# Performance work log

Hardware: AMD Instinct MI355X
Metric: run time of the kernel (lower is better)

The kernel has to match this reference:

```python
import jax, jax.numpy as jnp
import numpy as np

GAMMA = 5.0 / 3.0
SG = float(np.sqrt(GAMMA - 1.0))
NC, E, H = 1000000, 5, 32

def _csnd(rho, p):
    h = 1.0 + GAMMA / (GAMMA - 1.0) * p / rho
    return jnp.sqrt(GAMMA * p / (rho * h))

def _vstar_from_cs(cs, cs_a, v_a, wave_sign):
    # Marti-Muller relativistic rarefaction Riemann invariant
    ratio = ((SG - cs) / (SG + cs)) * ((SG + cs_a) / (SG - cs_a))
    A = ((1.0 + v_a) / (1.0 - v_a)) * ratio ** (-wave_sign * 2.0 / SG)
    return (A - 1.0) / (A + 1.0)

def _get_vel_raref(p, rho_a, p_a, v_a, wave_sign):
    rho = rho_a * (p / p_a) ** (1.0 / GAMMA)          # isentrope
    h = 1.0 + GAMMA / (GAMMA - 1.0) * p / rho
    cs = jnp.sqrt(GAMMA * p / (rho * h))
    vstar = _vstar_from_cs(cs, _csnd(rho_a, p_a), v_a, wave_sign)
    W = 1.0 / jnp.sqrt(1.0 - vstar ** 2)
    return rho, p / rho, h, cs, vstar, W

def _raref_solver(prims, sign):
    # state inside the rarefaction fan at xi = x/t = 0: v = sign*cs
    rho_a, p_a, v_a = prims[:, 0], prims[:, 1], prims[:, 2]
    cs_a = _csnd(rho_a, p_a)
    wave_sign = -float(sign)
    f = lambda cs: _vstar_from_cs(cs, cs_a, v_a, wave_sign) - sign * cs
    lo = jnp.full_like(rho_a, 1e-6)
    hi = jnp.full_like(rho_a, SG - 1e-6)
    flo = f(lo)
    for _ in range(40):  # fixed-count bisection, jit-safe
        mid = 0.5 * (lo + hi)
        fm = f(mid)
        same = jnp.sign(fm) == jnp.sign(flo)
        lo = jnp.where(same, mid, lo)
        flo = jnp.where(same, fm, flo)
        hi = jnp.where(same, hi, mid)
    cs = 0.5 * (lo + hi)
    h = (GAMMA - 1.0) / (GAMMA - 1.0 - cs ** 2)
    k = (h - 1.0) * (GAMMA - 1.0) / GAMMA              # p / rho
    rho = (k * rho_a ** GAMMA / p_a) ** (1.0 / (GAMMA - 1.0))
    return rho, k * rho, h, sign * cs

def setup_inputs():
    key = jax.random.key(0)
    ks = jax.random.split(key, 10)
    rho = 0.5 + jax.random.uniform(ks[0], (NC, 1, 2))
    p = 0.5 + jax.random.uniform(ks[1], (NC, 1, 2))
    v = 0.8 * (jax.random.uniform(ks[2], (NC, 1, 2)) - 0.5)
    P = jnp.concatenate([rho, p, v], axis=1)           # (NC,3,2)
    U = jax.random.normal(ks[3], (NC, 3, 2))
    F = jax.random.normal(ks[4], (NC, 3, 2))
    cmax = jax.random.uniform(ks[5], (NC,))
    cmin = -jax.random.uniform(ks[6], (NC,))
    s = lambda fan: 0.5 / np.sqrt(fan)
    W1 = jax.random.normal(ks[7], (E, H, 6)) * s(6)
    b1 = jnp.zeros((E, H))
    W2 = jax.random.normal(ks[8], (E, H, H)) * s(H)
    b2 = jnp.zeros((E, H))
    W3 = jax.random.normal(ks[9], (E, 1, H)) * s(H)
    b3 = jnp.zeros((E, 1))
    return {"P": P, "U": U, "F": F, "cmax": cmax, "cmin": cmin,
            "W1": W1, "b1": b1, "W2": W2, "b2": b2, "W3": W3, "b3": b3}

def _forward(P, U, F, cmax, cmin, W1, b1, W2, b2, W3, b3):
    rhoL, rhoR = P[:, 0, 0], P[:, 0, 1]
    pL, pR = P[:, 1, 0], P[:, 1, 1]
    vL, vR = P[:, 2, 0], P[:, 2, 1]
    # pressnet ensemble, batched over E instead of a Python loop
    x = jnp.concatenate([jnp.log(P[:, 0]), jnp.log(P[:, 1]), P[:, 2]], axis=1)  # (NC,6)
    h1 = jnp.tanh(jnp.einsum('nf,ehf->neh', x, W1) + b1)
    h2 = jnp.tanh(jnp.einsum('neh,egh->neg', h1, W2) + b2)
    xi = jax.nn.sigmoid(jnp.einsum('neh,eoh->neo', h2, W3) + b3)[..., 0]        # (NC,E)
    pressC = xi * jnp.minimum(pL, pR)[:, None]        # affine compactification [0, min(pL,pR)]
    rhoCLe, _, hCLe, csCLe, vstarLe, _ = _get_vel_raref(pressC, rhoL[:, None], pL[:, None], vL[:, None], -1.0)
    rhoCRe, _, hCRe, csCRe, vstarRe, _ = _get_vel_raref(pressC, rhoR[:, None], pR[:, None], vR[:, None], +1.0)
    best = jnp.argmin(jnp.abs(vstarLe - vstarRe), axis=1)
    pick = lambda a: jnp.take_along_axis(a, best[:, None], axis=1)[:, 0]
    pressCs = pick(pressC)
    rhoCL, hCL, csCL, vstarL = pick(rhoCLe), pick(hCLe), pick(csCLe), pick(vstarLe)
    rhoCR, hCR, csCR, vstarR = pick(rhoCRe), pick(hCRe), pick(csCRe), pick(vstarRe)
    csL, csR = _csnd(rhoL, pL), _csnd(rhoR, pR)
    lambdaC = 0.5 * (vstarR + vstarL)
    lambdaRL = (lambdaC - csCL) / (1.0 - lambdaC * csCL)
    lambdaL = (vL - csL) / (1.0 - vL * csL)
    lambdaRR = (lambdaC + csCR) / (1.0 + lambdaC * csCR)
    lambdaR = (vR + csR) / (1.0 + vR * csR)
    WC = 1.0 / jnp.sqrt(1.0 - lambdaC ** 2)
    densCL, densCR = WC * rhoCL, WC * rhoCR
    momCL = WC ** 2 * rhoCL * hCL * lambdaC
    momCR = WC ** 2 * rhoCR * hCR * lambdaC
    FCL = jnp.stack([densCL * lambdaC, densCL * (WC * hCL - 1.0) * lambdaC, momCL * lambdaC + pressCs], axis=1)
    FCR = jnp.stack([densCR * lambdaC, densCR * (WC * hCR - 1.0) * lambdaC, momCR * lambdaC + pressCs], axis=1)
    rho_RL, p_RL, h_RL, v_RL = _raref_solver(P[:, :3, 0], +1.0)
    rho_RR, p_RR, h_RR, v_RR = _raref_solver(P[:, :3, 1], -1.0)
    WRL = 1.0 / jnp.sqrt(1.0 - v_RL ** 2)
    WRR = 1.0 / jnp.sqrt(1.0 - v_RR ** 2)
    densRL, densRR = WRL * rho_RL, WRR * rho_RR
    momRL = WRL ** 2 * rho_RL * h_RL * v_RL
    momRR = WRR ** 2 * rho_RR * h_RR * v_RR
    FRL = jnp.stack([densRL * v_RL, densRL * (WRL * h_RL - 1.0) * v_RL, momRL * v_RL + p_RL], axis=1)
    FRR = jnp.stack([densRR * v_RR, densRR * (WRR * h_RR - 1.0) * v_RR, momRR * v_RR + p_RR], axis=1)
    fluxes = jnp.zeros_like(F[:, :, 0])
    sel = lambda m, val, cur: jnp.where(m[:, None], val, cur)
    fluxes = sel(lambdaL >= 0, F[:, :, 0], fluxes)
    fluxes = sel((lambdaL < 0) & (lambdaRL >= 0), FRL, fluxes)
    fluxes = sel((lambdaRL < 0) & (lambdaC > 0), FCL, fluxes)
    fluxes = sel((lambdaC <= 0) & (lambdaRR > 0), FCR, fluxes)
    fluxes = sel((lambdaRR <= 0) & (lambdaR > 0), FRR, fluxes)
    fluxes = sel(lambdaR <= 0, F[:, :, 1], fluxes)
    return fluxes

def reference(P, U, F, cmax, cmin, W1, b1, W2, b2, W3, b3):
    return _forward(P, U, F, cmax, cmin, W1, b1, W2, b2, W3, b3)
```

## Files before the change

kernel.cpp:

```cpp
#include <hip/hip_runtime.h>
#include <hip/hip_bf16.h>
#include <math.h>
#include <stdint.h>

namespace {

constexpr int NE  = 5;
constexpr int NH  = 32;
constexpr int BLK = 256;
constexpr int WPB = BLK / 64;

typedef __attribute__((ext_vector_type(8))) _Float16 half8;
typedef __attribute__((ext_vector_type(2))) __fp16   fp16x2;
typedef __attribute__((ext_vector_type(4))) float    f32x4;

union U4H8 { uint4 u; half8 h; };
union U1H2 { uint32_t u; fp16x2 h; };

__device__ __forceinline__ float bflo(uint32_t u){ return __uint_as_float(u << 16); }
__device__ __forceinline__ float bfhi(uint32_t u){ return __uint_as_float(u & 0xffff0000u); }
__device__ __forceinline__ float b2f(uint16_t u){ return __uint_as_float(((uint32_t)u) << 16); }

constexpr float GAM   = (float)(5.0 / 3.0);
constexpr float G1    = (float)(2.0 / 3.0);
constexpr float CP    = 2.5f;
constexpr float SGc   = (float)0.81649658092772603;
constexpr float E2SG  = (float)2.4494897427831781;
constexpr float LOG2E = 1.4426950408889634f;
constexpr float TLG   = 2.0f * LOG2E;

__device__ __forceinline__ float fexp2(float x){ return __builtin_amdgcn_exp2f(x); }
__device__ __forceinline__ float flog2(float x){ return __builtin_amdgcn_logf(x); }
__device__ __forceinline__ float frcp (float x){ return __builtin_amdgcn_rcpf(x); }
__device__ __forceinline__ float frsq (float x){ return __builtin_amdgcn_rsqf(x); }
__device__ __forceinline__ float fdiv (float a, float b){ return a * frcp(b); }

__device__ __forceinline__ float csnd_fast(float rho, float p){
    return sqrtf(GAM * p * frcp(rho + CP * p));
}

__device__ __forceinline__ uint32_t pk16(float a, float b){
    U1H2 x; x.h = __builtin_amdgcn_cvt_pkrtz(a, b); return x.u;
}
__device__ __forceinline__ uint32_t pkrtn(float a, float b){
    union { _Float16 h[2]; uint32_t u; } cv;
    cv.h[0] = (_Float16)a; cv.h[1] = (_Float16)b;
    return cv.u;
}

__device__ __forceinline__ int kxr(int r){ return (r ^ (r >> 2)) & 3; }

template<bool F32>
__device__ __forceinline__ float wload(const void* p, int idx){
    if constexpr (F32) return ((const float*)p)[idx];
    else               return b2f(((const uint16_t*)p)[idx]);
}

__device__ __forceinline__ void binv8(const float d[8], float i[8]){
    float P1 = d[0] * d[1], P2 = P1 * d[2], P3 = P2 * d[3];
    float P4 = P3 * d[4], P5 = P4 * d[5], P6 = P5 * d[6], P7 = P6 * d[7];
    float R = frcp(P7);
    i[7] = R * P6; R *= d[7];
    i[6] = R * P5; R *= d[6];
    i[5] = R * P4; R *= d[5];
    i[4] = R * P3; R *= d[4];
    i[3] = R * P2; R *= d[3];
    i[2] = R * P1; R *= d[2];
    i[1] = R * d[0];
    i[0] = R * d[1];
}

__device__ __forceinline__ void raref_solver2(float l2rhoL_, float pL_, float kNL,
                                              float l2rhoR_, float pR_, float kNR,
                                              float& rhoRL, float& pRL, float& hRL, float& vRL,
                                              float& rhoRR, float& pRR, float& hRR, float& vRR)
{
    float loL = 1e-6f, hiL = SGc - 1e-6f, csL = 0.40f;
    float loR = 1e-6f, hiR = SGc - 1e-6f, csR = 0.40f;
    #pragma unroll 1
    for(int it = 0; it < 12; ++it){
        float aL = SGc + csL, aR = SGc + csR;
        float Pa = aL * aR, Ra = frcp(Pa);
        float lrL = flog2((SGc - csL) * (Ra * aR));
        float lrR = flog2((SGc - csR) * (Ra * aL));
        float bL = 1.0f - csL, bR = 1.0f - csR;
        float Pb = bL * bR, Rb = frcp(Pb);
        float a2L = flog2((1.0f + csL) * (Rb * bR));
        float a2R = flog2((1.0f + csR) * (Rb * bL));
        float gL = fmaf(E2SG, lrL, kNL) - a2L;
        float gR = fmaf(-E2SG, lrR, kNR) + a2R;
        float d1L = (SGc - csL) * aL, d2L = bL * (1.0f + csL);
        float d1R = (SGc - csR) * aR, d2R = bR * (1.0f + csR);
        float numL = LOG2E * (-2.0f * SGc * E2SG * d2L - 2.0f * d1L);
        float numR = LOG2E * ( 2.0f * SGc * E2SG * d2R + 2.0f * d1R);
        float Pn = numL * numR, Rn = frcp(Pn);
        float csnL = csL - gL * d1L * d2L * (Rn * numR);
        float csnR = csR - gR * d1R * d2R * (Rn * numL);
        bool abL = (gL > 0.0f);
        bool abR = (gR < 0.0f);
        loL = abL ? csL : loL;  hiL = abL ? hiL : csL;
        loR = abR ? csR : loR;  hiR = abR ? hiR : csR;
        csnL = (csnL > loL && csnL < hiL) ? csnL : 0.5f * (loL + hiL);
        csnR = (csnR > loR && csnR < hiR) ? csnR : 0.5f * (loR + hiR);
        bool conv = (fabsf(csnL - csL) < 2e-7f) && (fabsf(csnR - csR) < 2e-7f);
        csL = csnL; csR = csnR;
        if(__all(conv)) break;
    }
    float e1L = G1 - csL * csL, e1R = G1 - csR * csR;
    float Pe = e1L * e1R, Re = frcp(Pe);
    hRL = G1 * (Re * e1R);  hRR = G1 * (Re * e1L);
    float kL = (hRL - 1.0f) * 0.4f, kR = (hRR - 1.0f) * 0.4f;
    float Pp = pL_ * pR_, Rp = frcp(Pp);
    float baseL = kL * fexp2(GAM * l2rhoL_) * (Rp * pR_);
    float baseR = kR * fexp2(GAM * l2rhoR_) * (Rp * pL_);
    rhoRL = baseL * sqrtf(baseL);
    rhoRR = baseR * sqrtf(baseR);
    pRL = kL * rhoRL;  pRR = kR * rhoRR;
    vRL = csL;  vRR = -csR;
}

template<bool F32>
__device__ __forceinline__ void cell_block(const void* Pp, const void* Fp,
                                           const void* W1p, const void* b1p,
                                           const void* W2p, const void* b2p,
                                           const void* W3p, const void* b3p,
                                           float* __restrict__ out, int nc,
                                           uint32_t* Hu ,
                                           uint32_t* sW1u ,
                                           uint32_t* sW2u ,
                                           float* sB1, float* sB2, float* sW3, float* sC)
{
    const int lane = threadIdx.x & 63;
    const int l16  = lane & 15;
    const int quad = lane >> 4;
    const int k16  = kxr(l16);
    const int sw   = quad ^ k16;

    for(int i = threadIdx.x; i < NE * NH * 16; i += BLK){
        int row = i >> 4, kp = i & 15;
        float f0 = wload<F32>(W2p, row * NH + 2 * kp) * TLG;
        float f1 = wload<F32>(W2p, row * NH + 2 * kp + 1) * TLG;
        int idx = (row << 4) | ((((kp >> 2) ^ kxr(row)) << 2) | (kp & 3));
        sW2u[idx] = pkrtn(f0, f1);
    }
    for(int i = threadIdx.x; i < NE * NH * 4; i += BLK){
        int row = i >> 2, kp = i & 3;
        int k0 = 2 * kp, k1 = 2 * kp + 1;
        float f0 = (k0 < 6) ? wload<F32>(W1p, row * 6 + k0) * ((k0 < 4) ? 2.0f : TLG) : 0.0f;
        float f1 = (k1 < 6) ? wload<F32>(W1p, row * 6 + k1) * ((k1 < 4) ? 2.0f : TLG) : 0.0f;
        sW1u[i] = pkrtn(f0, f1);
    }
    for(int i = threadIdx.x; i < NE * NH; i += BLK){
        sB1[i] = wload<F32>(b1p, i) * TLG;
        sB2[i] = wload<F32>(b2p, i) * TLG;
        sW3[i] = wload<F32>(W3p, i) * (-LOG2E);
    }
    if(threadIdx.x < NE){
        float s = wload<F32>(b3p, threadIdx.x) * (-LOG2E);
        for(int j = 0; j < NH; ++j)
            s += wload<F32>(W3p, threadIdx.x * NH + j) * (-LOG2E);
        sC[threadIdx.x] = s;
    }
    __syncthreads();

    const int n  = blockIdx.x * BLK + threadIdx.x;
    const bool valid = (n < nc);
    const int nn = valid ? n : 0;

    float rhoL, rhoR, pL, pR, vL, vR;
    if constexpr (F32){
        const float2* Pf = (const float2*)((const float*)Pp + (size_t)nn * 6);
        float2 a = Pf[0], b = Pf[1], c = Pf[2];
        rhoL = a.x; rhoR = a.y; pL = b.x; pR = b.y; vL = c.x; vR = c.y;
    } else {
        const uint32_t* P32 = (const uint32_t*)Pp;
        uint32_t pa = P32[nn * 3 + 0], pb = P32[nn * 3 + 1], pc = P32[nn * 3 + 2];
        rhoL = bflo(pa); rhoR = bfhi(pa);
        pL   = bflo(pb); pR   = bfhi(pb);
        vL   = bflo(pc); vR   = bfhi(pc);
    }

    float l2rhoL = flog2(rhoL), l2rhoR = flog2(rhoR);
    float l2pL   = flog2(pL),   l2pR   = flog2(pR);

    float csL = csnd_fast(rhoL, pL);
    float csR = csnd_fast(rhoR, pR);
    float pmin = fminf(pL, pR);
    float l2pmin = fminf(l2pL, l2pR);

    float lnraL = flog2((SGc + csL) * frcp(SGc - csL));
    float lnraR = flog2((SGc + csR) * frcp(SGc - csR));
    float lnvL  = flog2((1.0f + vL) * frcp(1.0f - vL));
    float lnvR  = flog2((1.0f + vR) * frcp(1.0f - vR));

    float kNL = fmaf( E2SG, lnraL, lnvL);
    float kNR = fmaf(-E2SG, lnraR, lnvR);

    float c6L = 0.6f * l2pL - l2rhoL;
    float c6R = 0.6f * l2pR - l2rhoR;
    float dLR = fexp2(c6R - c6L);

    U4H8 Bx[4];
    {
        uint32_t x01 = pk16(l2rhoL, l2rhoR);
        uint32_t x23 = pk16(l2pL, l2pR);
        uint32_t x45 = pk16(vL, vR);
        *(uint4*)&Hu[(lane << 4) + (k16 << 2)] = make_uint4(x01, x23, x45, 0u);
        #pragma unroll
        for(int t = 0; t < 4; ++t){
            uint4 b = *(const uint4*)&Hu[((t * 16 + l16) << 4) + (kxr(l16) << 2)];
            Bx[t].u = (quad == 0) ? b : make_uint4(0u, 0u, 0u, 0u);
        }
    }

    float bestd = 1e30f;
    float xaW = 0.f, porL = 1.f, csCL = 0.f, vstarL = 0.f;
    float porR = 1.f, csCR = 0.f, vstarR = 0.f;

    const int cpos0 = (((quad >> 1) ^ k16) << 2) + ((quad & 1) << 1);
    const int cpos1 = (((2 + (quad >> 1)) ^ k16) << 2) + ((quad & 1) << 1);

    #pragma unroll 1
    for(int e = 0; e < NE; ++e){
        U4H8 A1[2];
        #pragma unroll
        for(int m2 = 0; m2 < 2; ++m2){
            uint4 w = *(const uint4*)&sW1u[(e * NH + m2 * 16 + l16) << 2];
            A1[m2].u = (quad == 0) ? w : make_uint4(0u, 0u, 0u, 0u);
        }

        f32x4 acc1[2][4];
        #pragma unroll
        for(int m2 = 0; m2 < 2; ++m2){
            f32x4 bias = *(const f32x4*)&sB1[e * NH + m2 * 16 + quad * 4];
            #pragma unroll
            for(int t = 0; t < 4; ++t) acc1[m2][t] = bias;
        }
        #pragma unroll
        for(int t = 0; t < 4; ++t)
            #pragma unroll
            for(int m2 = 0; m2 < 2; ++m2)
                acc1[m2][t] = __builtin_amdgcn_mfma_f32_16x16x32_f16(A1[m2].h, Bx[t].h, acc1[m2][t], 0, 0, 0);

        #pragma unroll
        for(int t = 0; t < 4; ++t){
            float dv[8], iv[8];
            #pragma unroll
            for(int m2 = 0; m2 < 2; ++m2)
                #pragma unroll
                for(int r = 0; r < 4; ++r)
                    dv[m2 * 4 + r] = fexp2(acc1[m2][t][r]) + 1.0f;
            binv8(dv, iv);
            int c = t * 16 + l16;
            uint32_t u0 = pk16(fmaf(-2.0f, iv[0], 1.0f), fmaf(-2.0f, iv[1], 1.0f));
            uint32_t u1 = pk16(fmaf(-2.0f, iv[2], 1.0f), fmaf(-2.0f, iv[3], 1.0f));
            uint32_t u2 = pk16(fmaf(-2.0f, iv[4], 1.0f), fmaf(-2.0f, iv[5], 1.0f));
            uint32_t u3 = pk16(fmaf(-2.0f, iv[6], 1.0f), fmaf(-2.0f, iv[7], 1.0f));
            *(uint2*)&Hu[(c << 4) + cpos0] = make_uint2(u0, u1);
            *(uint2*)&Hu[(c << 4) + cpos1] = make_uint2(u2, u3);
        }

        U4H8 Ah[2];
        #pragma unroll
        for(int m2 = 0; m2 < 2; ++m2)
            Ah[m2].u = *(const uint4*)&sW2u[((e * NH + m2 * 16 + l16) << 4) + (sw << 2)];

        f32x4 acc[2][4];
        #pragma unroll
        for(int m2 = 0; m2 < 2; ++m2){
            f32x4 bias = *(const f32x4*)&sB2[e * NH + m2 * 16 + quad * 4];
            #pragma unroll
            for(int t = 0; t < 4; ++t) acc[m2][t] = bias;
        }

        #pragma unroll
        for(int t = 0; t < 4; ++t){
            int cell = t * 16 + l16;
            U4H8 Bh;
            Bh.u = *(const uint4*)&Hu[(cell << 4) + (sw << 2)];
            #pragma unroll
            for(int m2 = 0; m2 < 2; ++m2)
                acc[m2][t] = __builtin_amdgcn_mfma_f32_16x16x32_f16(Ah[m2].h, Bh.h, acc[m2][t], 0, 0, 0);
        }

        f32x4 w3v[2];
        #pragma unroll
        for(int m2 = 0; m2 < 2; ++m2)
            w3v[m2] = *(const f32x4*)&sW3[e * NH + m2 * 16 + quad * 4];
        float part[4];
        #pragma unroll
        for(int t = 0; t < 4; ++t){
            float dv[8], iv[8];
            #pragma unroll
            for(int m2 = 0; m2 < 2; ++m2)
                #pragma unroll
                for(int r = 0; r < 4; ++r)
                    dv[m2 * 4 + r] = fexp2(acc[m2][t][r]) + 1.0f;
            binv8(dv, iv);
            float s = 0.0f;
            #pragma unroll
            for(int m2 = 0; m2 < 2; ++m2)
                #pragma unroll
                for(int r = 0; r < 4; ++r)
                    s = fmaf(w3v[m2][r], iv[m2 * 4 + r], s);
            s += __shfl_xor(s, 16, 64);
            s += __shfl_xor(s, 32, 64);
            part[t] = s;
        }
        float p01 = (lane & 16) ? part[1] : part[0];
        float p23 = (lane & 16) ? part[3] : part[2];
        float partS = (lane & 32) ? p23 : p01;
        float xa = fmaf(-2.0f, partS, sC[e]);

        float E = fexp2(xa);
        float l2pC = l2pmin - flog2(1.0f + E);

        float porL_ = fexp2(fmaf(0.4f, l2pC, c6L));
        float porR_ = porL_ * dLR;
        float hL_ = fmaf(CP, porL_, 1.0f), hR_ = fmaf(CP, porR_, 1.0f);
        float Ph = hL_ * hR_, Rh = frcp(Ph);
        float csl = sqrtf(GAM * porL_ * (Rh * hR_));
        float csr = sqrtf(GAM * porR_ * (Rh * hL_));
        float dl = SGc + csl, dr = SGc + csr;
        float Pd = dl * dr, Rd = frcp(Pd);
        float lrl = flog2((SGc - csl) * (Rd * dr));
        float lrr = flog2((SGc - csr) * (Rd * dl));
        float AL = fexp2(fmaf( E2SG, lrl, kNL));
        float AR = fexp2(fmaf(-E2SG, lrr, kNR));
        float eL = AL + 1.0f, eR = AR + 1.0f;
        float Pa2 = eL * eR, Ra2 = frcp(Pa2);
        float vstL = 1.0f - 2.0f * (Ra2 * eR);
        float vstR = 1.0f - 2.0f * (Ra2 * eL);

        float d = fabsf(vstL - vstR);
        if(d < bestd){
            bestd = d;
            xaW = xa;
            porL = porL_; csCL = csl; vstarL = vstL;
            porR = porR_; csCR = csr; vstarR = vstR;
        }
    }

    float pressCs = pmin * frcp(1.0f + fexp2(xaW));
    float hCL = fmaf(CP, porL, 1.0f);
    float hCR = fmaf(CP, porR, 1.0f);
    float rhoCL = pressCs * frcp(porL);
    float rhoCR = pressCs * frcp(porR);

    float lambdaC  = 0.5f * (vstarR + vstarL);
    float lambdaRL = fdiv(lambdaC - csCL, 1.0f - lambdaC * csCL);
    float lambdaL  = fdiv(vL - csL,       1.0f - vL * csL);
    float lambdaRR = fdiv(lambdaC + csCR, 1.0f + lambdaC * csCR);
    float lambdaR  = fdiv(vR + csR,       1.0f + vR * csR);

    float WC = frsq(1.0f - lambdaC * lambdaC);
    float densCL = WC * rhoCL, densCR = WC * rhoCR;
    float momCL = WC * WC * rhoCL * hCL * lambdaC;
    float momCR = WC * WC * rhoCR * hCR * lambdaC;
    float FCL0 = densCL * lambdaC;
    float FCL1 = densCL * (WC * hCL - 1.0f) * lambdaC;
    float FCL2 = momCL * lambdaC + pressCs;
    float FCR0 = densCR * lambdaC;
    float FCR1 = densCR * (WC * hCR - 1.0f) * lambdaC;
    float FCR2 = momCR * lambdaC + pressCs;

    float rho_RL = 0.f, p_RL = 0.f, h_RL = 1.f, v_RL = 0.f;
    float rho_RR = 0.f, p_RR = 0.f, h_RR = 1.f, v_RR = 0.f;
    bool needL = (lambdaL < 0.0f)  && (lambdaRL >= 0.0f);
    bool needR = (lambdaRR <= 0.0f) && (lambdaR  >  0.0f);
    if(__any(needL || needR)){
        raref_solver2(l2rhoL, pL, kNL,
                      l2rhoR, pR, kNR,
                      rho_RL, p_RL, h_RL, v_RL,
                      rho_RR, p_RR, h_RR, v_RR);
    }

    float WRL = frsq(1.0f - v_RL * v_RL);
    float WRR = frsq(1.0f - v_RR * v_RR);
    float densRL = WRL * rho_RL, densRR = WRR * rho_RR;
    float momRL = WRL * WRL * rho_RL * h_RL * v_RL;
    float momRR = WRR * WRR * rho_RR * h_RR * v_RR;
    float FRL0 = densRL * v_RL;
    float FRL1 = densRL * (WRL * h_RL - 1.0f) * v_RL;
    float FRL2 = momRL * v_RL + p_RL;
    float FRR0 = densRR * v_RR;
    float FRR1 = densRR * (WRR * h_RR - 1.0f) * v_RR;
    float FRR2 = momRR * v_RR + p_RR;

    float FL0, FR0, FL1, FR1, FL2, FR2;
    if constexpr (F32){
        const float2* Ff = (const float2*)((const float*)Fp + (size_t)nn * 6);
        float2 fa = Ff[0], fb = Ff[1], fc = Ff[2];
        FL0 = fa.x; FR0 = fa.y; FL1 = fb.x; FR1 = fb.y; FL2 = fc.x; FR2 = fc.y;
    } else {
        const uint32_t* F32p = (const uint32_t*)Fp;
        uint32_t fa = F32p[nn * 3 + 0], fb = F32p[nn * 3 + 1], fc = F32p[nn * 3 + 2];
        FL0 = bflo(fa); FR0 = bfhi(fa);
        FL1 = bflo(fb); FR1 = bfhi(fb);
        FL2 = bflo(fc); FR2 = bfhi(fc);
    }

    float o0 = 0.f, o1 = 0.f, o2 = 0.f;
    if(lambdaL >= 0.0f)                        { o0 = FL0;  o1 = FL1;  o2 = FL2;  }
    if(lambdaL < 0.0f  && lambdaRL >= 0.0f)    { o0 = FRL0; o1 = FRL1; o2 = FRL2; }
    if(lambdaRL < 0.0f && lambdaC  >  0.0f)    { o0 = FCL0; o1 = FCL1; o2 = FCL2; }
    if(lambdaC  <= 0.0f && lambdaRR >  0.0f)   { o0 = FCR0; o1 = FCR1; o2 = FCR2; }
    if(lambdaRR <= 0.0f && lambdaR  >  0.0f)   { o0 = FRR0; o1 = FRR1; o2 = FRR2; }
    if(lambdaR  <= 0.0f)                       { o0 = FR0;  o1 = FR1;  o2 = FR2;  }

    if(valid){
        out[(size_t)n * 3 + 0] = o0;
        out[(size_t)n * 3 + 1] = o1;
        out[(size_t)n * 3 + 2] = o2;
    }
}

__global__ __launch_bounds__(BLK)
void solver_kernel(const void* __restrict__ Pp,
                   const void* __restrict__ Fp,
                   const void* __restrict__ W1p,
                   const void* __restrict__ b1p,
                   const void* __restrict__ W2p,
                   const void* __restrict__ b2p,
                   const void* __restrict__ W3p,
                   const void* __restrict__ b3p,
                   float* __restrict__ out, int nc)
{
    __shared__ __align__(16) uint32_t HuA[WPB][64 * 16];
    __shared__ __align__(16) uint32_t sW1u[NE * NH * 4];
    __shared__ __align__(16) uint32_t sW2u[NE * NH * 16];
    __shared__ __align__(16) float sB1[NE * NH];
    __shared__ __align__(16) float sB2[NE * NH];
    __shared__ __align__(16) float sW3[NE * NH];
    __shared__ __align__(16) float sC[NE];
    const int wv = threadIdx.x >> 6;

    const uint32_t* Pd = (const uint32_t*)Pp;
    int votes = 0;
    #pragma unroll
    for(int i = 0; i < 8; ++i){
        float tv = __uint_as_float(Pd[6 * i + 2]);
        votes += (tv >= 0.45f && tv <= 1.55f) ? 1 : 0;
    }
    if(votes >= 4)
        cell_block<true >(Pp, Fp, W1p, b1p, W2p, b2p, W3p, b3p, out, nc,
                          HuA[wv], sW1u, sW2u, sB1, sB2, sW3, sC);
    else
        cell_block<false>(Pp, Fp, W1p, b1p, W2p, b2p, W3p, b3p, out, nc,
                          HuA[wv], sW1u, sW2u, sB1, sB2, sW3, sC);
}

}

extern "C" void kernel_launch(void* const* d_in, const int* in_sizes, int n_in,
                              void* d_out, int out_size, void* d_ws, size_t ws_size,
                              hipStream_t stream) {
    const void* P  = d_in[0];
    const void* F  = d_in[2];
    const void* W1 = d_in[5];
    const void* b1 = d_in[6];
    const void* W2 = d_in[7];
    const void* b2 = d_in[8];
    const void* W3 = d_in[9];
    const void* b3 = d_in[10];
    float* out = (float*)d_out;

    int nc = in_sizes[0] / 6;
    dim3 grid((nc + BLK - 1) / BLK);
    hipLaunchKernelGGL(solver_kernel, grid, dim3(BLK), 0, stream,
                       P, F, W1, b1, W2, b2, W3, b3, out, nc);
}
```

Before: 207.3 us.

## Batch reciprocals, seed rarefaction Newton with closed-form guess, double block size

Replaces seven separate reciprocals after the star-state search with one batched inversion (binv8), which needs a single rcp plus extra multiplies. The rarefaction Newton solve now starts from an analytic rational approximation of the root instead of a fixed 0.40 guess, while keeping 12 iterations. The block size also goes from 256 to 512 threads. The batched inverse adds rounding and multiply chains, and the larger block may change occupancy.

```diff
diff --git a/kernel.cpp b/kernel.cpp
--- a/kernel.cpp
+++ b/kernel.cpp
@@ -7,7 +7,7 @@
 
 constexpr int NE  = 5;
 constexpr int NH  = 32;
-constexpr int BLK = 256;
+constexpr int BLK = 512;
 constexpr int WPB = BLK / 64;
 
 typedef __attribute__((ext_vector_type(8))) _Float16 half8;
@@ -27,13 +27,13 @@
 constexpr float SGc   = (float)0.81649658092772603;
 constexpr float E2SG  = (float)2.4494897427831781;
 constexpr float LOG2E = 1.4426950408889634f;
+constexpr float LN2   = 0.6931471805599453f;
 constexpr float TLG   = 2.0f * LOG2E;
 
 __device__ __forceinline__ float fexp2(float x){ return __builtin_amdgcn_exp2f(x); }
 __device__ __forceinline__ float flog2(float x){ return __builtin_amdgcn_logf(x); }
 __device__ __forceinline__ float frcp (float x){ return __builtin_amdgcn_rcpf(x); }
 __device__ __forceinline__ float frsq (float x){ return __builtin_amdgcn_rsqf(x); }
-__device__ __forceinline__ float fdiv (float a, float b){ return a * frcp(b); }
 
 __device__ __forceinline__ float csnd_fast(float rho, float p){
     return sqrtf(GAM * p * frcp(rho + CP * p));
@@ -75,8 +75,20 @@
                                               float& rhoRL, float& pRL, float& hRL, float& vRL,
                                               float& rhoRR, float& pRR, float& hRR, float& vRR)
 {
-    float loL = 1e-6f, hiL = SGc - 1e-6f, csL = 0.40f;
-    float loR = 1e-6f, hiR = SGc - 1e-6f, csR = 0.40f;
+    float loL = 1e-6f, hiL = SGc - 1e-6f;
+    float loR = 1e-6f, hiR = SGc - 1e-6f;
+
+    float KpL = kNL * (0.5f * LN2);
+    float KpR = (-kNR) * (0.5f * LN2);
+    float c0L = fminf(KpL * 0.25f, SGc - 1e-6f);
+    float c0R = fminf(KpR * 0.25f, SGc - 1e-6f);
+    float qL = c0L * c0L, qR = c0R * c0R;
+    float denL = fmaf(qL, fmaf(1.55f, qL, 1.8333333f), 4.0f);
+    float denR = fmaf(qR, fmaf(1.55f, qR, 1.8333333f), 4.0f);
+    float Pg = denL * denR, Rg = frcp(Pg);
+    float csL = fminf(fmaxf(KpL * (Rg * denR), 1e-6f), SGc - 1e-6f);
+    float csR = fminf(fmaxf(KpR * (Rg * denL), 1e-6f), SGc - 1e-6f);
+
     #pragma unroll 1
     for(int it = 0; it < 12; ++it){
         float aL = SGc + csL, aR = SGc + csR;
@@ -341,17 +353,26 @@
         }
     }
 
-    float pressCs = pmin * frcp(1.0f + fexp2(xaW));
+    float lambdaC = 0.5f * (vstarR + vstarL);
+    float dv[8], iv[8];
+    dv[0] = 1.0f + fexp2(xaW);
+    dv[1] = porL;
+    dv[2] = porR;
+    dv[3] = 1.0f - lambdaC * csCL;
+    dv[4] = 1.0f - vL * csL;
+    dv[5] = 1.0f + lambdaC * csCR;
+    dv[6] = 1.0f + vR * csR;
+    dv[7] = 1.0f;
+    binv8(dv, iv);
+    float pressCs = pmin * iv[0];
     float hCL = fmaf(CP, porL, 1.0f);
     float hCR = fmaf(CP, porR, 1.0f);
-    float rhoCL = pressCs * frcp(porL);
-    float rhoCR = pressCs * frcp(porR);
-
-    float lambdaC  = 0.5f * (vstarR + vstarL);
-    float lambdaRL = fdiv(lambdaC - csCL, 1.0f - lambdaC * csCL);
-    float lambdaL  = fdiv(vL - csL,       1.0f - vL * csL);
-    float lambdaRR = fdiv(lambdaC + csCR, 1.0f + lambdaC * csCR);
-    float lambdaR  = fdiv(vR + csR,       1.0f + vR * csR);
+    float rhoCL = pressCs * iv[1];
+    float rhoCR = pressCs * iv[2];
+    float lambdaRL = (lambdaC - csCL) * iv[3];
+    float lambdaL  = (vL - csL)       * iv[4];
+    float lambdaRR = (lambdaC + csCR) * iv[5];
+    float lambdaR  = (vR + csR)       * iv[6];
 
     float WC = frsq(1.0f - lambdaC * lambdaC);
     float densCL = WC * rhoCL, densCR = WC * rhoCR;
```

Measured after the change: 196.5 us. 1.05x faster.
